# Kernel tuning notes

Measured on AMD Instinct MI355X. Metric: run time of the kernel, lower is better.

The kernel has to match this reference:

```python
import jax, jax.numpy as jnp
import numpy as np

N_NODES = 50000
N_EDGES = 800000
H_DIM = 128


def setup_inputs() -> dict:
    key = jax.random.key(0)
    ks = jax.random.split(key, 12)
    h = jax.random.normal(ks[0], (N_NODES, H_DIM), dtype=jnp.float32)
    feat_ct = jax.random.normal(ks[1], (N_EDGES, 1), dtype=jnp.float32)
    feat_cb = jax.random.normal(ks[2], (N_EDGES, 1), dtype=jnp.float32)
    src_ct = jax.random.randint(ks[3], (N_EDGES,), 0, N_NODES, dtype=jnp.int32)
    dst_ct = jax.random.randint(ks[4], (N_EDGES,), 0, N_NODES, dtype=jnp.int32)
    src_cb = jax.random.randint(ks[5], (N_EDGES,), 0, N_NODES, dtype=jnp.int32)
    dst_cb = jax.random.randint(ks[6], (N_EDGES,), 0, N_NODES, dtype=jnp.int32)
    # torch Linear(2h, h): weight [h, 2h]; store transposed [2h, h], kaiming-ish scale
    scale = 1.0 / np.sqrt(2 * H_DIM)
    W0 = jax.random.uniform(ks[7], (2 * H_DIM, H_DIM), minval=-scale, maxval=scale, dtype=jnp.float32)
    b0 = jnp.zeros((H_DIM,), dtype=jnp.float32)
    W1 = jax.random.uniform(ks[8], (2 * H_DIM, H_DIM), minval=-scale, maxval=scale, dtype=jnp.float32)
    b1 = jnp.zeros((H_DIM,), dtype=jnp.float32)
    return {"h": h, "feat_ct": feat_ct, "feat_cb": feat_cb,
            "src_ct": src_ct, "dst_ct": dst_ct, "src_cb": src_cb, "dst_cb": dst_cb,
            "W0": W0, "b0": b0, "W1": W1, "b1": b1}


def _agg(h, feat, src, dst, n):
    # e_mul_u: per-edge scalar weight * source node feature, sum-reduced to dst
    return jax.ops.segment_sum(feat * h[src], dst, num_segments=n)


def reference(h, feat_ct, feat_cb, src_ct, dst_ct, src_cb, dst_cb, W0, b0, W1, b1):
    n = h.shape[0]
    for W, b in ((W0, b0), (W1, b1)):
        m_ct = _agg(h, feat_ct, src_ct, dst_ct, n)   # [N, h]
        m_cb = _agg(h, feat_cb, src_cb, dst_cb, n)   # [N, h]
        t = jnp.concatenate([m_ct, m_cb], axis=-1)   # [N, 2h]
        h_ = jax.nn.gelu(t @ W + b, approximate=False)
        h = h + h_                                    # residual update of node 'h'
    return h
```

## Files before the change

kernel.cpp:

```cpp
#include <hip/hip_runtime.h>
#include <math.h>

#define HDIM 128
#define CH 4096
typedef unsigned int uint;
using short8 = __attribute__((ext_vector_type(8))) short;
using f32x4  = __attribute__((ext_vector_type(4))) float;

__device__ __forceinline__ uint pack_bf16x2(float a, float b) {
    uint ua = __float_as_uint(a), ub = __float_as_uint(b);
    ua = (ua + 0x7fffu + ((ua >> 16) & 1u)) >> 16;
    ub = (ub + 0x7fffu + ((ub >> 16) & 1u)) & 0xffff0000u;
    return ua | ub;
}
__device__ __forceinline__ unsigned short pack_bf16(float a) {
    uint ua = __float_as_uint(a);
    return (unsigned short)((ua + 0x7fffu + ((ua >> 16) & 1u)) >> 16);
}

__global__ __launch_bounds__(256) void prep_kernel(
    const float* __restrict__ h, uint* __restrict__ hb, int n_pairs,
    const float* __restrict__ W0, const float* __restrict__ W1,
    unsigned short* __restrict__ Wt0, unsigned short* __restrict__ Wt1)
{
    const int total = n_pairs + 2 * 32768;
    for (int i = blockIdx.x * 256 + threadIdx.x; i < total; i += gridDim.x * 256) {
        if (i < n_pairs) {
            float2 v = reinterpret_cast<const float2*>(h)[i];
            hb[i] = pack_bf16x2(v.x, v.y);
        } else {
            int t = i - n_pairs;
            const float* W = (t < 32768) ? W0 : W1;
            unsigned short* Wt = (t < 32768) ? Wt0 : Wt1;
            int j = t & 32767;
            int c = j >> 8, k = j & 255;
            Wt[j] = pack_bf16(W[k * HDIM + c]);
        }
    }
}

__global__ __launch_bounds__(256) void histc_kernel(
    const int* __restrict__ dst_ct, int* __restrict__ cntm_ct, int n_ct, int nv_ct,
    const int* __restrict__ dst_cb, int* __restrict__ cntm_cb, int n_cb, int nv_cb,
    int nbuckets)
{
    __shared__ int lh[512];
    const bool cb = ((int)blockIdx.x >= nv_ct);
    const int vb = cb ? blockIdx.x - nv_ct : blockIdx.x;
    const int* dst = cb ? dst_cb : dst_ct;
    int* cntm      = cb ? cntm_cb : cntm_ct;
    const int n  = cb ? n_cb : n_ct;
    const int NV = cb ? nv_cb : nv_ct;
    for (int j = threadIdx.x; j < 512; j += 256) lh[j] = 0;
    __syncthreads();
    const int e0 = vb << 12;
    const int e1 = min(n, e0 + CH);
    for (int i = e0 + threadIdx.x; i < e1; i += 256)
        atomicAdd(&lh[dst[i] >> 7], 1);
    __syncthreads();
    for (int j = threadIdx.x; j < nbuckets; j += 256)
        cntm[j * NV + vb] = lh[j];
}

__global__ __launch_bounds__(256) void scanA_kernel(
    int* __restrict__ cntm_ct, int* __restrict__ tot_ct, int nv_ct,
    int* __restrict__ cntm_cb, int* __restrict__ tot_cb, int nv_cb,
    int nbuckets)
{
    __shared__ int buf[256];
    const bool cb = ((int)blockIdx.x >= nbuckets);
    const int b = cb ? blockIdx.x - nbuckets : blockIdx.x;
    int* cntm = cb ? cntm_cb : cntm_ct;
    int* tot  = cb ? tot_cb : tot_ct;
    const int NV = cb ? nv_cb : nv_ct;
    const int t = threadIdx.x;
    int base = 0;
    for (int t0 = 0; t0 < NV; t0 += 256) {
        const int idx = t0 + t;
        const int v = (idx < NV) ? cntm[b * NV + idx] : 0;
        buf[t] = v;
        __syncthreads();
        #pragma unroll
        for (int off = 1; off < 256; off <<= 1) {
            int x = (t >= off) ? buf[t - off] : 0;
            __syncthreads();
            buf[t] += x;
            __syncthreads();
        }
        if (idx < NV) cntm[b * NV + idx] = base + buf[t] - v;
        base += buf[255];
        __syncthreads();
    }
    if (t == 0) tot[b] = base;
}

__global__ __launch_bounds__(1024) void scanB_kernel(
    const int* __restrict__ tot_ct, int* __restrict__ bkt_ct,
    const int* __restrict__ tot_cb, int* __restrict__ bkt_cb, int nbuckets)
{
    __shared__ int buf[1024];
    const int* tot = blockIdx.x ? tot_cb : tot_ct;
    int* bkt       = blockIdx.x ? bkt_cb : bkt_ct;
    const int t = threadIdx.x;
    const int v = (t < nbuckets) ? tot[t] : 0;
    buf[t] = v;
    __syncthreads();
    #pragma unroll
    for (int off = 1; off < 1024; off <<= 1) {
        int x = (t >= off) ? buf[t - off] : 0;
        __syncthreads();
        buf[t] += x;
        __syncthreads();
    }
    if (t < nbuckets) bkt[t] = buf[t] - v;
    if (t == nbuckets - 1) bkt[nbuckets] = buf[t];
}

__global__ __launch_bounds__(256) void part_kernel(
    const int* __restrict__ dst_ct, const int* __restrict__ src_ct,
    const float* __restrict__ feat_ct, const int* __restrict__ off_ct,
    const int* __restrict__ bkt_ct, int2* __restrict__ ebkt_ct, int n_ct, int nv_ct,
    const int* __restrict__ dst_cb, const int* __restrict__ src_cb,
    const float* __restrict__ feat_cb, const int* __restrict__ off_cb,
    const int* __restrict__ bkt_cb, int2* __restrict__ ebkt_cb, int n_cb, int nv_cb,
    int nbuckets)
{
    __shared__ int cur[512];
    const bool cb = ((int)blockIdx.x >= nv_ct);
    const int vb = cb ? blockIdx.x - nv_ct : blockIdx.x;
    const int* dst    = cb ? dst_cb : dst_ct;
    const int* srcp   = cb ? src_cb : src_ct;
    const float* feat = cb ? feat_cb : feat_ct;
    const int* off    = cb ? off_cb : off_ct;
    const int* bkt    = cb ? bkt_cb : bkt_ct;
    int2* ebkt        = cb ? ebkt_cb : ebkt_ct;
    const int n  = cb ? n_cb : n_ct;
    const int NV = cb ? nv_cb : nv_ct;
    for (int j = threadIdx.x; j < nbuckets; j += 256)
        cur[j] = off[j * NV + vb] + bkt[j];
    __syncthreads();
    const int e0 = vb << 12;
    const int e1 = min(n, e0 + CH);
    for (int i = e0 + threadIdx.x; i < e1; i += 256) {
        int d = dst[i];
        int p = atomicAdd(&cur[d >> 7], 1);
        ebkt[p] = make_int2((srcp[i] & 0xFFFF) | ((d & 127) << 16),
                            __float_as_int(feat[i]));
    }
}

__global__ __launch_bounds__(256) void sortb_kernel(
    const int2* __restrict__ ebkt_ct, const int* __restrict__ bkt_ct,
    const int2* __restrict__ ebkt_cb, const int* __restrict__ bkt_cb,
    int2* __restrict__ ecsr_ct, int2* __restrict__ ecsr_cb,
    int* __restrict__ rowptr_ct, int* __restrict__ rowptr_cb,
    int n_nodes, int nbuckets)
{
    __shared__ int cnt[128];
    __shared__ int pref[128];
    const int b = blockIdx.x >> 1;
    const bool cb = blockIdx.x & 1;
    const int2* ebkt = cb ? ebkt_cb : ebkt_ct;
    const int* bkt   = cb ? bkt_cb : bkt_ct;
    int2* ecsr       = cb ? ecsr_cb : ecsr_ct;
    int* rowptr      = cb ? rowptr_cb : rowptr_ct;
    const int t = threadIdx.x;
    const int beg = bkt[b], end = bkt[b + 1];

    if (t < 128) cnt[t] = 0;
    __syncthreads();
    for (int i = beg + t; i < end; i += 256)
        atomicAdd(&cnt[((uint)ebkt[i].x) >> 16], 1);
    __syncthreads();
    if (t < 128) pref[t] = cnt[t];
    __syncthreads();
    #pragma unroll
    for (int off = 1; off < 128; off <<= 1) {
        int v = 0;
        if (t < 128 && t >= off) v = pref[t - off];
        __syncthreads();
        if (t < 128) pref[t] += v;
        __syncthreads();
    }
    if (t < 128) {
        int n0 = b * 128;
        int base = beg + pref[t] - cnt[t];
        if (n0 + t < n_nodes) rowptr[n0 + t] = base;
        cnt[t] = base;
    }
    if (b == nbuckets - 1 && t == 0) rowptr[n_nodes] = end;
    __syncthreads();
    for (int i = beg + t; i < end; i += 256) {
        int2 r = ebkt[i];
        int d = ((uint)r.x) >> 16;
        int p = atomicAdd(&cnt[d], 1);
        ecsr[p] = r;
    }
}

__global__ __launch_bounds__(256) void csr_gather_bf16_kernel(
    const uint2* __restrict__ hb,
    const int* __restrict__ rp_ct, const int2* __restrict__ e_ct,
    const int* __restrict__ rp_cb, const int2* __restrict__ e_cb,
    uint2* __restrict__ mct, uint2* __restrict__ mcb, int n_nodes)
{
    const int lane = threadIdx.x & 63;
    const int half = lane >> 5;
    const int sub  = lane & 31;
    const int wave = (blockIdx.x * 256 + threadIdx.x) >> 6;
    const int nwaves = (gridDim.x * 256) >> 6;
    const int total = 2 * n_nodes;
    for (int v = wave; v < total; v += nwaves) {
        const bool cbt = (v >= n_nodes);
        const int n = cbt ? (v - n_nodes) : v;
        const int* rp    = cbt ? rp_cb : rp_ct;
        const int2* ecsr = cbt ? e_cb : e_ct;
        uint2* m = cbt ? mcb : mct;
        const int beg = rp[n], end = rp[n + 1];
        float a0 = 0.f, a1 = 0.f, a2 = 0.f, a3 = 0.f;
        for (int i0 = beg; i0 < end; i0 += 64) {
            const int cnt = min(64, end - i0);
            int s = 0; float f = 0.0f;
            if (lane < cnt) {
                int2 e = ecsr[i0 + lane];
                s = e.x & 0xFFFF;
                f = __int_as_float(e.y);
            }
            const int npair = (cnt + 1) >> 1;
            #pragma unroll 4
            for (int jj = 0; jj < npair; ++jj) {
                int idx = jj * 2 + half;
                int   sj = __shfl(s, idx);
                float fj = __shfl(f, idx);
                uint2 hv = hb[(size_t)sj * 32 + sub];
                a0 = fmaf(fj, __uint_as_float(hv.x << 16),         a0);
                a1 = fmaf(fj, __uint_as_float(hv.x & 0xffff0000u), a1);
                a2 = fmaf(fj, __uint_as_float(hv.y << 16),         a2);
                a3 = fmaf(fj, __uint_as_float(hv.y & 0xffff0000u), a3);
            }
        }
        a0 += __shfl_xor(a0, 32);
        a1 += __shfl_xor(a1, 32);
        a2 += __shfl_xor(a2, 32);
        a3 += __shfl_xor(a3, 32);
        if (half == 0)
            m[(size_t)n * 32 + sub] = make_uint2(pack_bf16x2(a0, a1),
                                                 pack_bf16x2(a2, a3));
    }
}

__global__ __launch_bounds__(256) void gemm_mfma_kernel(
    const unsigned short* __restrict__ mct, const unsigned short* __restrict__ mcb,
    const unsigned short* __restrict__ Wt, const float* __restrict__ bias,
    const float* __restrict__ h_in, float* __restrict__ h_out,
    unsigned short* __restrict__ hb_out, int n_nodes, int write_hb)
{
    const int base = blockIdx.x * 128;
    const int lane = threadIdx.x & 63;
    const int wid  = threadIdx.x >> 6;
    const int lr = lane & 15, lg = lane >> 4;
    const int row0 = base + wid * 32;

    f32x4 acc[2][8];
    #pragma unroll
    for (int mi = 0; mi < 2; ++mi)
        #pragma unroll
        for (int ni = 0; ni < 8; ++ni)
            acc[mi][ni] = (f32x4){0.f, 0.f, 0.f, 0.f};

    const int last = (base + 128 > n_nodes);

    #pragma unroll
    for (int ks = 0; ks < 8; ++ks) {
        const int koff = ks * 32 + lg * 8;
        short8 a[2], b[8];
        #pragma unroll
        for (int mi = 0; mi < 2; ++mi) {
            int node = row0 + mi * 16 + lr;
            if (last && node >= n_nodes) node = n_nodes - 1;
            const unsigned short* srcp = (koff < 128)
                ? (mct + (size_t)node * HDIM + koff)
                : (mcb + (size_t)node * HDIM + (koff - 128));
            a[mi] = *reinterpret_cast<const short8*>(srcp);
        }
        #pragma unroll
        for (int ni = 0; ni < 8; ++ni) {
            int col = ni * 16 + lr;
            b[ni] = *reinterpret_cast<const short8*>(Wt + (size_t)col * 256 + koff);
        }
        #pragma unroll
        for (int mi = 0; mi < 2; ++mi)
            #pragma unroll
            for (int ni = 0; ni < 8; ++ni)
                acc[mi][ni] = __builtin_amdgcn_mfma_f32_16x16x32_bf16(
                    a[mi], b[ni], acc[mi][ni], 0, 0, 0);
    }

    #pragma unroll
    for (int mi = 0; mi < 2; ++mi) {
        #pragma unroll
        for (int ni = 0; ni < 8; ++ni) {
            const int col = ni * 16 + lr;
            const float bc = bias[col];
            #pragma unroll
            for (int j = 0; j < 4; ++j) {
                int node = row0 + mi * 16 + lg * 4 + j;
                if (node < n_nodes) {
                    float x = acc[mi][ni][j] + bc;
                    float g = 0.5f * x * (1.0f + erff(x * 0.70710678118654752f));
                    float o = h_in[(size_t)node * HDIM + col] + g;
                    h_out[(size_t)node * HDIM + col] = o;
                    if (write_hb)
                        hb_out[(size_t)node * HDIM + col] = pack_bf16(o);
                }
            }
        }
    }
}

__global__ __launch_bounds__(256) void edge_agg_kernel(
    const float* __restrict__ h, const float* __restrict__ feat,
    const int* __restrict__ src, const int* __restrict__ dst,
    float* __restrict__ m, int n_edges)
{
    long long tid = (long long)blockIdx.x * 256 + threadIdx.x;
    int e = (int)(tid >> 5);
    if (e >= n_edges) return;
    int q = (int)(tid & 31);
    float f = feat[e];
    size_t s = (size_t)src[e] * HDIM;
    size_t d = (size_t)dst[e] * HDIM;
    float4 v = reinterpret_cast<const float4*>(h + s)[q];
    float* mp = m + d + (size_t)q * 4;
    unsafeAtomicAdd(mp + 0, f * v.x);
    unsafeAtomicAdd(mp + 1, f * v.y);
    unsafeAtomicAdd(mp + 2, f * v.z);
    unsafeAtomicAdd(mp + 3, f * v.w);
}

__global__ __launch_bounds__(256) void gemm_gelu_res_kernel(
    const float* __restrict__ mct, const float* __restrict__ mcb,
    const float* __restrict__ W, const float* __restrict__ bias,
    const float* __restrict__ h_in, float* __restrict__ h_out, int n_nodes)
{
    __shared__ float Wl[256 * HDIM];
    __shared__ float trow[8][2 * HDIM];
    for (int i = threadIdx.x; i < 256 * HDIM; i += 256)
        Wl[i] = W[i];
    const int c = threadIdx.x & 127;
    const int g = threadIdx.x >> 7;
    const float bc = bias[c];
    __syncthreads();
    const int niter = (n_nodes + 7) >> 3;
    for (int it = blockIdx.x; it < niter; it += gridDim.x) {
        __syncthreads();
        for (int j = threadIdx.x; j < 8 * 256; j += 256) {
            int nn = j >> 8;
            int k  = j & 255;
            long long node = (long long)it * 8 + nn;
            float val = 0.0f;
            if (node < n_nodes)
                val = (k < HDIM) ? mct[node * HDIM + k]
                                 : mcb[node * HDIM + (k - HDIM)];
            trow[nn][k] = val;
        }
        __syncthreads();
        const float* t0 = trow[g * 4 + 0];
        const float* t1 = trow[g * 4 + 1];
        const float* t2 = trow[g * 4 + 2];
        const float* t3 = trow[g * 4 + 3];
        float a0 = bc, a1 = bc, a2 = bc, a3 = bc;
        #pragma unroll 8
        for (int k = 0; k < 256; ++k) {
            float w = Wl[k * HDIM + c];
            a0 = fmaf(t0[k], w, a0);
            a1 = fmaf(t1[k], w, a1);
            a2 = fmaf(t2[k], w, a2);
            a3 = fmaf(t3[k], w, a3);
        }
        float accs[4] = {a0, a1, a2, a3};
        #pragma unroll
        for (int j = 0; j < 4; ++j) {
            long long node = (long long)it * 8 + g * 4 + j;
            if (node < n_nodes) {
                float x = accs[j];
                float gl = 0.5f * x * (1.0f + erff(x * 0.70710678118654752f));
                h_out[node * HDIM + c] = h_in[node * HDIM + c] + gl;
            }
        }
    }
}

extern "C" void kernel_launch(void* const* d_in, const int* in_sizes, int n_in,
                              void* d_out, int out_size, void* d_ws, size_t ws_size,
                              hipStream_t stream)
{
    const float* h0      = (const float*)d_in[0];
    const float* feat_ct = (const float*)d_in[1];
    const float* feat_cb = (const float*)d_in[2];
    const int*   src_ct  = (const int*)d_in[3];
    const int*   dst_ct  = (const int*)d_in[4];
    const int*   src_cb  = (const int*)d_in[5];
    const int*   dst_cb  = (const int*)d_in[6];
    const float* W0      = (const float*)d_in[7];
    const float* b0      = (const float*)d_in[8];
    const float* W1      = (const float*)d_in[9];
    const float* b1      = (const float*)d_in[10];

    const int n_nodes    = in_sizes[0] / HDIM;
    const int n_edges_ct = in_sizes[3];
    const int n_edges_cb = in_sizes[5];
    float* out = (float*)d_out;

    const int nbuckets = (n_nodes + 127) >> 7;
    const int nv_ct = (n_edges_ct + CH - 1) / CH;
    const int nv_cb = (n_edges_cb + CH - 1) / CH;

    char* p = (char*)d_ws;
    auto take = [&](size_t bytes) -> char* {
        char* r = p;
        p += (bytes + 255) & ~(size_t)255;
        return r;
    };
    unsigned short* hb   = (unsigned short*)take((size_t)n_nodes * HDIM * 2);
    unsigned short* mctb = (unsigned short*)take((size_t)n_nodes * HDIM * 2);
    unsigned short* mcbb = (unsigned short*)take((size_t)n_nodes * HDIM * 2);
    unsigned short* Wt0  = (unsigned short*)take(32768 * 2);
    unsigned short* Wt1  = (unsigned short*)take(32768 * 2);
    int* cntm_ct = (int*)take((size_t)nbuckets * nv_ct * 4);
    int* cntm_cb = (int*)take((size_t)nbuckets * nv_cb * 4);
    int* tot_ct  = (int*)take((size_t)nbuckets * 4);
    int* tot_cb  = (int*)take((size_t)nbuckets * 4);
    int* bkt_ct  = (int*)take(((size_t)nbuckets + 1) * 4);
    int* bkt_cb  = (int*)take(((size_t)nbuckets + 1) * 4);
    int* rowptr_ct = (int*)take(((size_t)n_nodes + 1) * 4);
    int* rowptr_cb = (int*)take(((size_t)n_nodes + 1) * 4);
    int2* ecsr_ct = (int2*)take((size_t)n_edges_ct * 8);
    int2* ecsr_cb = (int2*)take((size_t)n_edges_cb * 8);
    const size_t need_bytes = (size_t)(p - (char*)d_ws);
    int2* ebkt_ct = (int2*)mctb;
    int2* ebkt_cb = (int2*)mcbb;

    const bool ebkt_fits =
        ((size_t)n_edges_ct * 8 <= (size_t)n_nodes * HDIM * 2) &&
        ((size_t)n_edges_cb * 8 <= (size_t)n_nodes * HDIM * 2);

    if (ws_size >= need_bytes && n_nodes <= 65536 && ebkt_fits) {
        prep_kernel<<<2048, 256, 0, stream>>>(
            h0, (uint*)hb, n_nodes * (HDIM / 2), W0, W1, Wt0, Wt1);
        histc_kernel<<<nv_ct + nv_cb, 256, 0, stream>>>(
            dst_ct, cntm_ct, n_edges_ct, nv_ct,
            dst_cb, cntm_cb, n_edges_cb, nv_cb, nbuckets);
        scanA_kernel<<<nbuckets * 2, 256, 0, stream>>>(
            cntm_ct, tot_ct, nv_ct, cntm_cb, tot_cb, nv_cb, nbuckets);
        scanB_kernel<<<2, 1024, 0, stream>>>(
            tot_ct, bkt_ct, tot_cb, bkt_cb, nbuckets);
        part_kernel<<<nv_ct + nv_cb, 256, 0, stream>>>(
            dst_ct, src_ct, feat_ct, cntm_ct, bkt_ct, ebkt_ct, n_edges_ct, nv_ct,
            dst_cb, src_cb, feat_cb, cntm_cb, bkt_cb, ebkt_cb, n_edges_cb, nv_cb,
            nbuckets);
        sortb_kernel<<<nbuckets * 2, 256, 0, stream>>>(
            ebkt_ct, bkt_ct, ebkt_cb, bkt_cb, ecsr_ct, ecsr_cb,
            rowptr_ct, rowptr_cb, n_nodes, nbuckets);
        const int gemm_blocks = (n_nodes + 127) / 128;
        const float* hin = h0;
        for (int layer = 0; layer < 2; ++layer) {
            csr_gather_bf16_kernel<<<2048, 256, 0, stream>>>(
                (const uint2*)hb, rowptr_ct, ecsr_ct, rowptr_cb, ecsr_cb,
                (uint2*)mctb, (uint2*)mcbb, n_nodes);
            gemm_mfma_kernel<<<gemm_blocks, 256, 0, stream>>>(
                mctb, mcbb, layer ? Wt1 : Wt0, layer ? b1 : b0,
                hin, out, hb, n_nodes, layer == 0 ? 1 : 0);
            hin = out;
        }
    } else {
        float* mct = (float*)d_ws;
        float* mcb = mct + (size_t)n_nodes * HDIM;
        const size_t mbytes = (size_t)n_nodes * HDIM * sizeof(float) * 2;
        const int agg_blocks_ct = (int)(((long long)n_edges_ct * 32 + 255) / 256);
        const int agg_blocks_cb = (int)(((long long)n_edges_cb * 32 + 255) / 256);
        const float* hcur = h0;
        for (int layer = 0; layer < 2; ++layer) {
            hipMemsetAsync(d_ws, 0, mbytes, stream);
            edge_agg_kernel<<<agg_blocks_ct, 256, 0, stream>>>(
                hcur, feat_ct, src_ct, dst_ct, mct, n_edges_ct);
            edge_agg_kernel<<<agg_blocks_cb, 256, 0, stream>>>(
                hcur, feat_cb, src_cb, dst_cb, mcb, n_edges_cb);
            gemm_gelu_res_kernel<<<256, 256, 0, stream>>>(
                mct, mcb, layer ? W1 : W0, layer ? b1 : b0, hcur, out, n_nodes);
            hcur = out;
        }
    }
}
```

Measured before the change: 279.8 us.

## Slice bf16 node features into column-major chunks for cache-local gather

The bf16 copy of h is re-laid out as four column slices of 32 features each, stored contiguously per slice. The prep kernel and the GEMM epilogue now write this sliced layout. The CSR gather assigns each block one slice, and each wave processes 8 edges at a time with 8 lanes per edge. The aim is a smaller per-slice working set (about 3.2MB) that fits better in L2/MALL for the random source gathers. In exchange, each edge list is read four times, loads become 64-byte segments, and the gather needs extra shuffle-reduction steps.

```diff
diff --git a/kernel.cpp b/kernel.cpp
--- a/kernel.cpp
+++ b/kernel.cpp
@@ -19,17 +19,22 @@
 }
 
 __global__ __launch_bounds__(256) void prep_kernel(
-    const float* __restrict__ h, uint* __restrict__ hb, int n_pairs,
+    const float* __restrict__ h, uint* __restrict__ hb, int n_nodes,
     const float* __restrict__ W0, const float* __restrict__ W1,
     unsigned short* __restrict__ Wt0, unsigned short* __restrict__ Wt1)
 {
-    const int total = n_pairs + 2 * 32768;
+    const int N16 = n_nodes * 16;
+    const int t0 = n_nodes * 64;
+    const int total = t0 + 2 * 32768;
     for (int i = blockIdx.x * 256 + threadIdx.x; i < total; i += gridDim.x * 256) {
-        if (i < n_pairs) {
-            float2 v = reinterpret_cast<const float2*>(h)[i];
+        if (i < t0) {
+            int s = i / N16;
+            int r = i - s * N16;
+            int n = r >> 4, q = r & 15;
+            float2 v = reinterpret_cast<const float2*>(h)[(size_t)n * 64 + s * 16 + q];
             hb[i] = pack_bf16x2(v.x, v.y);
         } else {
-            int t = i - n_pairs;
+            int t = i - t0;
             const float* W = (t < 32768) ? W0 : W1;
             unsigned short* Wt = (t < 32768) ? Wt0 : Wt1;
             int j = t & 32767;
@@ -205,12 +210,15 @@
     uint2* __restrict__ mct, uint2* __restrict__ mcb, int n_nodes)
 {
     const int lane = threadIdx.x & 63;
-    const int half = lane >> 5;
-    const int sub  = lane & 31;
-    const int wave = (blockIdx.x * 256 + threadIdx.x) >> 6;
-    const int nwaves = (gridDim.x * 256) >> 6;
+    const int eg = lane >> 3;
+    const int q  = lane & 7;
+    const int slice = blockIdx.x & 3;
+    const int wid = threadIdx.x >> 6;
+    const int u0 = (blockIdx.x >> 2) * 4 + wid;
+    const int ustride = (gridDim.x >> 2) * 4;
+    const uint2* hbs = hb + (size_t)slice * ((size_t)n_nodes * 8);
     const int total = 2 * n_nodes;
-    for (int v = wave; v < total; v += nwaves) {
+    for (int v = u0; v < total; v += ustride) {
         const bool cbt = (v >= n_nodes);
         const int n = cbt ? (v - n_nodes) : v;
         const int* rp    = cbt ? rp_cb : rp_ct;
@@ -226,26 +234,28 @@
                 s = e.x & 0xFFFF;
                 f = __int_as_float(e.y);
             }
-            const int npair = (cnt + 1) >> 1;
+            const int nsub = (cnt + 7) >> 3;
             #pragma unroll 4
-            for (int jj = 0; jj < npair; ++jj) {
-                int idx = jj * 2 + half;
+            for (int jj = 0; jj < nsub; ++jj) {
+                int idx = jj * 8 + eg;
                 int   sj = __shfl(s, idx);
                 float fj = __shfl(f, idx);
-                uint2 hv = hb[(size_t)sj * 32 + sub];
+                uint2 hv = hbs[(size_t)sj * 8 + q];
                 a0 = fmaf(fj, __uint_as_float(hv.x << 16),         a0);
                 a1 = fmaf(fj, __uint_as_float(hv.x & 0xffff0000u), a1);
                 a2 = fmaf(fj, __uint_as_float(hv.y << 16),         a2);
                 a3 = fmaf(fj, __uint_as_float(hv.y & 0xffff0000u), a3);
             }
         }
-        a0 += __shfl_xor(a0, 32);
-        a1 += __shfl_xor(a1, 32);
-        a2 += __shfl_xor(a2, 32);
-        a3 += __shfl_xor(a3, 32);
-        if (half == 0)
-            m[(size_t)n * 32 + sub] = make_uint2(pack_bf16x2(a0, a1),
-                                                 pack_bf16x2(a2, a3));
+        a0 += __shfl_xor(a0, 8);  a1 += __shfl_xor(a1, 8);
+        a2 += __shfl_xor(a2, 8);  a3 += __shfl_xor(a3, 8);
+        a0 += __shfl_xor(a0, 16); a1 += __shfl_xor(a1, 16);
+        a2 += __shfl_xor(a2, 16); a3 += __shfl_xor(a3, 16);
+        a0 += __shfl_xor(a0, 32); a1 += __shfl_xor(a1, 32);
+        a2 += __shfl_xor(a2, 32); a3 += __shfl_xor(a3, 32);
+        if (eg == 0)
+            m[(size_t)n * 32 + slice * 8 + q] =
+                make_uint2(pack_bf16x2(a0, a1), pack_bf16x2(a2, a3));
     }
 }
 
@@ -310,8 +320,10 @@
                     float g = 0.5f * x * (1.0f + erff(x * 0.70710678118654752f));
                     float o = h_in[(size_t)node * HDIM + col] + g;
                     h_out[(size_t)node * HDIM + col] = o;
-                    if (write_hb)
-                        hb_out[(size_t)node * HDIM + col] = pack_bf16(o);
+                    if (write_hb) {
+                        hb_out[(size_t)(col >> 5) * ((size_t)n_nodes * 32)
+                               + (size_t)node * 32 + (col & 31)] = pack_bf16(o);
+                    }
                 }
             }
         }
@@ -447,7 +459,7 @@
 
     if (ws_size >= need_bytes && n_nodes <= 65536 && ebkt_fits) {
         prep_kernel<<<2048, 256, 0, stream>>>(
-            h0, (uint*)hb, n_nodes * (HDIM / 2), W0, W1, Wt0, Wt1);
+            h0, (uint*)hb, n_nodes, W0, W1, Wt0, Wt1);
         histc_kernel<<<nv_ct + nv_cb, 256, 0, stream>>>(
             dst_ct, cntm_ct, n_edges_ct, nv_ct,
             dst_cb, cntm_cb, n_edges_cb, nv_cb, nbuckets);
```

Result: slower. 359.3 us (+28.4%).

## Fuse prep with histogram, pack CSR edges to 32 bits, keep residual h in bf16

Applied to the files above, without the earlier changes.

Merges the bf16 conversion kernel into the histogram kernel by block ranges, saving a launch. CSR edge records shrink from 8 to 4 bytes by storing the source index and a bf16 edge weight, which cuts gather traffic. The first layer no longer writes fp32 h; the second layer takes its residual from the bf16 copy. This removes one fp32 write and read but loses precision in the residual and in the edge weights.

```diff
diff --git a/kernel.cpp b/kernel.cpp
--- a/kernel.cpp
+++ b/kernel.cpp
@@ -18,35 +18,37 @@
     return (unsigned short)((ua + 0x7fffu + ((ua >> 16) & 1u)) >> 16);
 }
 
-__global__ __launch_bounds__(256) void prep_kernel(
+__global__ __launch_bounds__(256) void prep_hist_kernel(
     const float* __restrict__ h, uint* __restrict__ hb, int n_pairs,
     const float* __restrict__ W0, const float* __restrict__ W1,
-    unsigned short* __restrict__ Wt0, unsigned short* __restrict__ Wt1)
-{
-    const int total = n_pairs + 2 * 32768;
-    for (int i = blockIdx.x * 256 + threadIdx.x; i < total; i += gridDim.x * 256) {
-        if (i < n_pairs) {
-            float2 v = reinterpret_cast<const float2*>(h)[i];
-            hb[i] = pack_bf16x2(v.x, v.y);
-        } else {
-            int t = i - n_pairs;
-            const float* W = (t < 32768) ? W0 : W1;
-            unsigned short* Wt = (t < 32768) ? Wt0 : Wt1;
-            int j = t & 32767;
-            int c = j >> 8, k = j & 255;
-            Wt[j] = pack_bf16(W[k * HDIM + c]);
-        }
-    }
-}
-
-__global__ __launch_bounds__(256) void histc_kernel(
+    unsigned short* __restrict__ Wt0, unsigned short* __restrict__ Wt1,
+    int conv_blocks,
     const int* __restrict__ dst_ct, int* __restrict__ cntm_ct, int n_ct, int nv_ct,
     const int* __restrict__ dst_cb, int* __restrict__ cntm_cb, int n_cb, int nv_cb,
     int nbuckets)
 {
+    if ((int)blockIdx.x < conv_blocks) {
+        const int total = n_pairs + 2 * 32768;
+        for (int i = blockIdx.x * 256 + threadIdx.x; i < total;
+             i += conv_blocks * 256) {
+            if (i < n_pairs) {
+                float2 v = reinterpret_cast<const float2*>(h)[i];
+                hb[i] = pack_bf16x2(v.x, v.y);
+            } else {
+                int t = i - n_pairs;
+                const float* W = (t < 32768) ? W0 : W1;
+                unsigned short* Wt = (t < 32768) ? Wt0 : Wt1;
+                int j = t & 32767;
+                int c = j >> 8, k = j & 255;
+                Wt[j] = pack_bf16(W[k * HDIM + c]);
+            }
+        }
+        return;
+    }
     __shared__ int lh[512];
-    const bool cb = ((int)blockIdx.x >= nv_ct);
-    const int vb = cb ? blockIdx.x - nv_ct : blockIdx.x;
+    const int hb_id = blockIdx.x - conv_blocks;
+    const bool cb = (hb_id >= nv_ct);
+    const int vb = cb ? hb_id - nv_ct : hb_id;
     const int* dst = cb ? dst_cb : dst_ct;
     int* cntm      = cb ? cntm_cb : cntm_ct;
     const int n  = cb ? n_cb : n_ct;
@@ -152,7 +154,7 @@
 __global__ __launch_bounds__(256) void sortb_kernel(
     const int2* __restrict__ ebkt_ct, const int* __restrict__ bkt_ct,
     const int2* __restrict__ ebkt_cb, const int* __restrict__ bkt_cb,
-    int2* __restrict__ ecsr_ct, int2* __restrict__ ecsr_cb,
+    uint* __restrict__ ecsr_ct, uint* __restrict__ ecsr_cb,
     int* __restrict__ rowptr_ct, int* __restrict__ rowptr_cb,
     int n_nodes, int nbuckets)
 {
@@ -162,7 +164,7 @@
     const bool cb = blockIdx.x & 1;
     const int2* ebkt = cb ? ebkt_cb : ebkt_ct;
     const int* bkt   = cb ? bkt_cb : bkt_ct;
-    int2* ecsr       = cb ? ecsr_cb : ecsr_ct;
+    uint* ecsr       = cb ? ecsr_cb : ecsr_ct;
     int* rowptr      = cb ? rowptr_cb : rowptr_ct;
     const int t = threadIdx.x;
     const int beg = bkt[b], end = bkt[b + 1];
@@ -194,14 +196,15 @@
         int2 r = ebkt[i];
         int d = ((uint)r.x) >> 16;
         int p = atomicAdd(&cnt[d], 1);
-        ecsr[p] = r;
+        ecsr[p] = (uint)(r.x & 0xFFFF) |
+                  ((uint)pack_bf16(__int_as_float(r.y)) << 16);
     }
 }
 
 __global__ __launch_bounds__(256) void csr_gather_bf16_kernel(
     const uint2* __restrict__ hb,
-    const int* __restrict__ rp_ct, const int2* __restrict__ e_ct,
-    const int* __restrict__ rp_cb, const int2* __restrict__ e_cb,
+    const int* __restrict__ rp_ct, const uint* __restrict__ e_ct,
+    const int* __restrict__ rp_cb, const uint* __restrict__ e_cb,
     uint2* __restrict__ mct, uint2* __restrict__ mcb, int n_nodes)
 {
     const int lane = threadIdx.x & 63;
@@ -214,7 +217,7 @@
         const bool cbt = (v >= n_nodes);
         const int n = cbt ? (v - n_nodes) : v;
         const int* rp    = cbt ? rp_cb : rp_ct;
-        const int2* ecsr = cbt ? e_cb : e_ct;
+        const uint* ecsr = cbt ? e_cb : e_ct;
         uint2* m = cbt ? mcb : mct;
         const int beg = rp[n], end = rp[n + 1];
         float a0 = 0.f, a1 = 0.f, a2 = 0.f, a3 = 0.f;
@@ -222,9 +225,9 @@
             const int cnt = min(64, end - i0);
             int s = 0; float f = 0.0f;
             if (lane < cnt) {
-                int2 e = ecsr[i0 + lane];
-                s = e.x & 0xFFFF;
-                f = __int_as_float(e.y);
+                uint e = ecsr[i0 + lane];
+                s = (int)(e & 0xFFFFu);
+                f = __uint_as_float(e & 0xffff0000u);
             }
             const int npair = (cnt + 1) >> 1;
             #pragma unroll 4
@@ -252,8 +255,9 @@
 __global__ __launch_bounds__(256) void gemm_mfma_kernel(
     const unsigned short* __restrict__ mct, const unsigned short* __restrict__ mcb,
     const unsigned short* __restrict__ Wt, const float* __restrict__ bias,
-    const float* __restrict__ h_in, float* __restrict__ h_out,
-    unsigned short* __restrict__ hb_out, int n_nodes, int write_hb)
+    const float* __restrict__ h_in, const unsigned short* __restrict__ hb_in,
+    float* __restrict__ h_out, unsigned short* __restrict__ hb_out,
+    int n_nodes, int mode)
 {
     const int base = blockIdx.x * 128;
     const int lane = threadIdx.x & 63;
@@ -308,10 +312,14 @@
                 if (node < n_nodes) {
                     float x = acc[mi][ni][j] + bc;
                     float g = 0.5f * x * (1.0f + erff(x * 0.70710678118654752f));
-                    float o = h_in[(size_t)node * HDIM + col] + g;
-                    h_out[(size_t)node * HDIM + col] = o;
-                    if (write_hb)
-                        hb_out[(size_t)node * HDIM + col] = pack_bf16(o);
+                    const size_t idx = (size_t)node * HDIM + col;
+                    if (mode == 0) {
+                        float o = h_in[idx] + g;
+                        hb_out[idx] = pack_bf16(o);
+                    } else {
+                        float hprev = __uint_as_float((uint)hb_in[idx] << 16);
+                        h_out[idx] = hprev + g;
+                    }
                 }
             }
         }
@@ -435,8 +443,8 @@
     int* bkt_cb  = (int*)take(((size_t)nbuckets + 1) * 4);
     int* rowptr_ct = (int*)take(((size_t)n_nodes + 1) * 4);
     int* rowptr_cb = (int*)take(((size_t)n_nodes + 1) * 4);
-    int2* ecsr_ct = (int2*)take((size_t)n_edges_ct * 8);
-    int2* ecsr_cb = (int2*)take((size_t)n_edges_cb * 8);
+    uint* ecsr_ct = (uint*)take((size_t)n_edges_ct * 4);
+    uint* ecsr_cb = (uint*)take((size_t)n_edges_cb * 4);
     const size_t need_bytes = (size_t)(p - (char*)d_ws);
     int2* ebkt_ct = (int2*)mctb;
     int2* ebkt_cb = (int2*)mcbb;
@@ -446,9 +454,9 @@
         ((size_t)n_edges_cb * 8 <= (size_t)n_nodes * HDIM * 2);
 
     if (ws_size >= need_bytes && n_nodes <= 65536 && ebkt_fits) {
-        prep_kernel<<<2048, 256, 0, stream>>>(
-            h0, (uint*)hb, n_nodes * (HDIM / 2), W0, W1, Wt0, Wt1);
-        histc_kernel<<<nv_ct + nv_cb, 256, 0, stream>>>(
+        const int conv_blocks = 2048;
+        prep_hist_kernel<<<conv_blocks + nv_ct + nv_cb, 256, 0, stream>>>(
+            h0, (uint*)hb, n_nodes * (HDIM / 2), W0, W1, Wt0, Wt1, conv_blocks,
             dst_ct, cntm_ct, n_edges_ct, nv_ct,
             dst_cb, cntm_cb, n_edges_cb, nv_cb, nbuckets);
         scanA_kernel<<<nbuckets * 2, 256, 0, stream>>>(
@@ -463,16 +471,16 @@
             ebkt_ct, bkt_ct, ebkt_cb, bkt_cb, ecsr_ct, ecsr_cb,
             rowptr_ct, rowptr_cb, n_nodes, nbuckets);
         const int gemm_blocks = (n_nodes + 127) / 128;
-        const float* hin = h0;
-        for (int layer = 0; layer < 2; ++layer) {
-            csr_gather_bf16_kernel<<<2048, 256, 0, stream>>>(
-                (const uint2*)hb, rowptr_ct, ecsr_ct, rowptr_cb, ecsr_cb,
-                (uint2*)mctb, (uint2*)mcbb, n_nodes);
-            gemm_mfma_kernel<<<gemm_blocks, 256, 0, stream>>>(
-                mctb, mcbb, layer ? Wt1 : Wt0, layer ? b1 : b0,
-                hin, out, hb, n_nodes, layer == 0 ? 1 : 0);
-            hin = out;
-        }
+        csr_gather_bf16_kernel<<<2048, 256, 0, stream>>>(
+            (const uint2*)hb, rowptr_ct, ecsr_ct, rowptr_cb, ecsr_cb,
+            (uint2*)mctb, (uint2*)mcbb, n_nodes);
+        gemm_mfma_kernel<<<gemm_blocks, 256, 0, stream>>>(
+            mctb, mcbb, Wt0, b0, h0, hb, out, hb, n_nodes, 0);
+        csr_gather_bf16_kernel<<<2048, 256, 0, stream>>>(
+            (const uint2*)hb, rowptr_ct, ecsr_ct, rowptr_cb, ecsr_cb,
+            (uint2*)mctb, (uint2*)mcbb, n_nodes);
+        gemm_mfma_kernel<<<gemm_blocks, 256, 0, stream>>>(
+            mctb, mcbb, Wt1, b1, h0, hb, out, hb, n_nodes, 1);
     } else {
         float* mct = (float*)d_ws;
         float* mcb = mct + (size_t)n_nodes * HDIM;
```

Measured after the change: 279.1 us. No clear change (-0.3%).
